# Performance work log

Hardware: AMD Instinct MI355X
Metric: run time of the kernel (lower is better)

Reference implementation:

```python
import jax, jax.numpy as jnp
import numpy as np

N_NODES = 100000
N_EDGES = 3200000
N_GRAPHS = 128
HIDDEN = 128
DEPTH = 3


def setup_inputs() -> dict:
    key = jax.random.key(0)
    ks = jax.random.split(key, 12)
    x = jax.random.normal(ks[0], (N_NODES, 1), dtype=jnp.float32)
    edge_index = jax.random.randint(ks[1], (2, N_EDGES), 0, N_NODES, dtype=jnp.int64)
    batch = jnp.sort(jax.random.randint(ks[2], (N_NODES,), 0, N_GRAPHS, dtype=jnp.int64))
    s = 1.0 / np.sqrt(HIDDEN)
    return {
        "x": x,
        "edge_index": edge_index,
        "batch": batch,
        "W_emb": jax.random.normal(ks[3], (1, HIDDEN), dtype=jnp.float32),
        "b_emb": jax.random.normal(ks[4], (HIDDEN,), dtype=jnp.float32) * 0.01,
        "W_gnn": jax.random.normal(ks[5], (DEPTH, HIDDEN, HIDDEN), dtype=jnp.float32) * s,
        "b_gnn": jax.random.normal(ks[6], (DEPTH, HIDDEN), dtype=jnp.float32) * 0.01,
        "W_c1": jax.random.normal(ks[7], (HIDDEN, HIDDEN // 2), dtype=jnp.float32) * s,
        "b_c1": jax.random.normal(ks[8], (HIDDEN // 2,), dtype=jnp.float32) * 0.01,
        "W_c2": jax.random.normal(ks[9], (HIDDEN // 2, 1), dtype=jnp.float32) * s,
        "b_c2": jax.random.normal(ks[10], (1,), dtype=jnp.float32) * 0.01,
    }


def reference(x, edge_index, batch, W_emb, b_emb, W_gnn, b_gnn, W_c1, b_c1, W_c2, b_c2):
    # --- GCN normalization (self-loops + symmetric deg^-1/2) ---
    loop = jnp.arange(N_NODES, dtype=edge_index.dtype)
    row = jnp.concatenate([edge_index[0], loop])  # source nodes
    col = jnp.concatenate([edge_index[1], loop])  # target nodes
    deg = jax.ops.segment_sum(jnp.ones_like(col, dtype=jnp.float32), col, num_segments=N_NODES)
    dinv = jnp.where(deg > 0, jax.lax.rsqrt(jnp.maximum(deg, 1.0)), 0.0)
    norm = dinv[row] * dinv[col]  # [E+N]

    # --- node embedding ---
    h = x @ W_emb + b_emb  # [N, H]

    # --- GCN layers: linear -> gather -> normalize -> scatter-add -> bias -> relu ---
    for l in range(DEPTH):
        h_lin = h @ W_gnn[l]                       # [N, H]
        msgs = h_lin[row] * norm[:, None]          # [E+N, H]
        agg = jax.ops.segment_sum(msgs, col, num_segments=N_NODES)
        h = jax.nn.relu(agg + b_gnn[l])

    # --- global mean pool per graph ---
    counts = jax.ops.segment_sum(jnp.ones((N_NODES,), jnp.float32), batch, num_segments=N_GRAPHS)
    sums = jax.ops.segment_sum(h, batch, num_segments=N_GRAPHS)
    g = sums / jnp.maximum(counts, 1.0)[:, None]   # [G, H]

    # --- classifier (dropout is identity in eval) ---
    z = jax.nn.relu(g @ W_c1 + b_c1)
    out = jax.nn.sigmoid(z @ W_c2 + b_c2)          # [G, 1]
    return out.squeeze(-1)                          # [G]
```

## Files before the change

### kernel.cpp

```cpp
#include <hip/hip_runtime.h>
#include <math.h>

#define HID 128
#define CAP 96
#define TILE 8192
#define WSH 9
#define BUKCAP 24576

typedef unsigned int uint;
typedef unsigned short ushort;
typedef float f32x2 __attribute__((ext_vector_type(2)));
typedef float f32x4 __attribute__((ext_vector_type(4)));
typedef short bf16x8 __attribute__((ext_vector_type(8)));

__device__ inline ushort f2bf(float f) {
    uint u = __float_as_uint(f);
    return (ushort)((u + 0x7fffu + ((u >> 16) & 1u)) >> 16);
}
__device__ inline float bflo(uint u) { return __uint_as_float(u << 16); }
__device__ inline float bfhi(uint u) { return __uint_as_float(u & 0xffff0000u); }
__device__ inline uint packbf(float a, float b) {
    return (uint)f2bf(a) | ((uint)f2bf(b) << 16);
}
__device__ inline bf16x8 as_bf16x8(uint4 u) {
    union { uint4 a; bf16x8 b; } c;
    c.a = u;
    return c.b;
}

__device__ inline f32x2 fp8lo(uint q) { return __builtin_amdgcn_cvt_pk_f32_fp8(q, false); }
__device__ inline f32x2 fp8hi(uint q) { return __builtin_amdgcn_cvt_pk_f32_fp8(q, true); }
__device__ inline uint pack4fp8(float a, float b, float c, float d) {
    int t = __builtin_amdgcn_cvt_pk_fp8_f32(a, b, 0, false);
    return (uint)__builtin_amdgcn_cvt_pk_fp8_f32(c, d, t, true);
}


__global__ void __launch_bounds__(256) k_part(const int* __restrict__ row,
                                              const int* __restrict__ col,
                                              int* __restrict__ bukCur,
                                              uint* __restrict__ recs, int E) {
    __shared__ int hist[256];
    __shared__ int hist2[256];
    __shared__ uint base[256];
    int t = threadIdx.x;
    hist[t] = 0;
    hist2[t] = 0;
    __syncthreads();
    int i0 = blockIdx.x * TILE;
    int i1 = min(E, i0 + TILE);
    for (int i = i0 + t; i < i1; i += 256) {
        int b = col[i] >> WSH;
        atomicAdd(&hist[b], 1);
    }
    __syncthreads();
    if (hist[t] > 0) base[t] = (uint)atomicAdd(&bukCur[t], hist[t]);
    __syncthreads();
    for (int i = i0 + t; i < i1; i += 256) {
        int c = col[i];
        int b = c >> WSH;
        uint p = (uint)atomicAdd(&hist2[b], 1);
        uint idx = base[b] + p;
        if (idx < BUKCAP)
            recs[(size_t)b * BUKCAP + idx] = (uint)row[i] | ((uint)(c & 511) << 17);
    }
}

__global__ void __launch_bounds__(256) k_fbin(const uint* __restrict__ recs,
                                              const int* __restrict__ bukCur,
                                              int* __restrict__ cnt,
                                              int* __restrict__ ebin, int N) {
    __shared__ int lcnt[512];
    int b = blockIdx.x;
    int t = threadIdx.x;
    lcnt[t] = 0;
    lcnt[t + 256] = 0;
    __syncthreads();
    int n = min(bukCur[b], BUKCAP);
    const uint* rp = recs + (size_t)b * BUKCAP;
    int cbase = b << WSH;
    for (int j = t; j < n; j += 256) {
        uint u = rp[j];
        int r = (int)(u & 0x1FFFFu);
        int cl = (int)(u >> 17);
        int p = atomicAdd(&lcnt[cl], 1);
        if (p < CAP) ebin[(size_t)(cbase + cl) * CAP + p] = r;
    }
    __syncthreads();
    int c0 = cbase + t;
    if (c0 < N) cnt[c0] = lcnt[t];
    int c1 = cbase + t + 256;
    if (c1 < N) cnt[c1] = lcnt[t + 256];
}

__global__ void k_prep(const int* __restrict__ cnt, const float* __restrict__ x,
                       float* __restrict__ dinv, float2* __restrict__ pk0, int N) {
    int i = blockIdx.x * blockDim.x + threadIdx.x;
    if (i < N) {
        float d = rsqrtf((float)cnt[i] + 1.0f);
        dinv[i] = d;
        pk0[i] = make_float2(d, d * x[i]);
    }
}


__global__ void k_uv(const float* __restrict__ W_emb, const float* __restrict__ b_emb,
                     const float* __restrict__ W0, float* __restrict__ u, float* __restrict__ v) {
    int j = threadIdx.x;
    float su = 0.f, sv = 0.f;
    for (int k = 0; k < HID; ++k) {
        float w = W0[k * HID + j];
        su = fmaf(W_emb[k], w, su);
        sv = fmaf(b_emb[k], w, sv);
    }
    u[j] = su;
    v[j] = sv;
}

__global__ void k_sagg(const int* __restrict__ cnt, const int* __restrict__ ebin,
                       const float* __restrict__ x, const float* __restrict__ dinv,
                       const float2* __restrict__ pk0,
                       float* __restrict__ s0, float* __restrict__ s1, int N) {
    int c = blockIdx.x * blockDim.x + threadIdx.x;
    if (c >= N) return;
    float dc = dinv[c];
    float A = 0.f, B = 0.f;
    int n = min(cnt[c], CAP);
    const int* bp = ebin + (size_t)c * CAP;
    int k = 0;
    for (; k + 4 <= n; k += 4) {
        float2 p0 = pk0[bp[k]], p1 = pk0[bp[k + 1]];
        float2 p2 = pk0[bp[k + 2]], p3 = pk0[bp[k + 3]];
        A += (p0.x + p1.x) + (p2.x + p3.x);
        B += (p0.y + p1.y) + (p2.y + p3.y);
    }
    for (; k < n; ++k) {
        float2 p = pk0[bp[k]];
        A += p.x;
        B += p.y;
    }
    float d2 = dc * dc;
    s0[c] = fmaf(dc, A, d2);
    s1[c] = fmaf(dc, B, d2 * x[c]);
}

__global__ void k_h1(const float* __restrict__ s0, const float* __restrict__ s1,
                     const float* __restrict__ u, const float* __restrict__ v,
                     const float* __restrict__ b0, const float* __restrict__ dinv,
                     uint* __restrict__ g8, int total) {
    int idx = blockIdx.x * blockDim.x + threadIdx.x;
    if (idx >= total) return;
    int c = idx >> 5, j = (idx & 31) * 4;
    float t0 = s1[c], t1 = s0[c];
    float dc = dinv[c];
    float v0 = fmaxf(fmaf(t0, u[j + 0], fmaf(t1, v[j + 0], b0[j + 0])), 0.f);
    float v1 = fmaxf(fmaf(t0, u[j + 1], fmaf(t1, v[j + 1], b0[j + 1])), 0.f);
    float v2 = fmaxf(fmaf(t0, u[j + 2], fmaf(t1, v[j + 2], b0[j + 2])), 0.f);
    float v3 = fmaxf(fmaf(t0, u[j + 3], fmaf(t1, v[j + 3], b0[j + 3])), 0.f);
    g8[idx] = pack4fp8(dc * v0, dc * v1, dc * v2, dc * v3);
}


__global__ void __launch_bounds__(256) k_agg(const int* __restrict__ cnt,
                                             const int* __restrict__ ebin,
                                             const float* __restrict__ dinv,
                                             const uint* __restrict__ g8,
                                             uint* __restrict__ a, int N) {
    int wave = (blockIdx.x * 256 + threadIdx.x) >> 6;
    int lane = threadIdx.x & 63;
    if (wave >= N) return;
    int c = wave;
    int sl = lane & 31;
    int halfid = lane >> 5;
    bool h0 = (halfid == 0);

    f32x2 acc01, acc23;
    {
        uint sq = g8[c * 32 + sl];
        f32x2 lo = fp8lo(sq), hi = fp8hi(sq);
        f32x2 z = {0.f, 0.f};
        acc01 = h0 ? lo : z;
        acc23 = h0 ? hi : z;
    }

    int n = min(cnt[c], CAP);
    const int* __restrict__ bp = ebin + (size_t)c * CAP;
    for (int base = 0; base < n; base += 64) {
        int cw = min(n - base, 64);
        int r = 0;
        if (lane < cw) r = bp[base + lane];
        int j = 0;
        for (; j + 8 <= cw; j += 8) {
            int rA = __shfl(r, j + halfid);
            int rB = __shfl(r, j + 2 + halfid);
            int rC = __shfl(r, j + 4 + halfid);
            int rD = __shfl(r, j + 6 + halfid);
            uint qA = g8[rA * 32 + sl];
            uint qB = g8[rB * 32 + sl];
            uint qC = g8[rC * 32 + sl];
            uint qD = g8[rD * 32 + sl];
            acc01 += fp8lo(qA); acc23 += fp8hi(qA);
            acc01 += fp8lo(qB); acc23 += fp8hi(qB);
            acc01 += fp8lo(qC); acc23 += fp8hi(qC);
            acc01 += fp8lo(qD); acc23 += fp8hi(qD);
        }
        for (; j + 2 <= cw; j += 2) {
            int rA = __shfl(r, j + halfid);
            uint qA = g8[rA * 32 + sl];
            acc01 += fp8lo(qA); acc23 += fp8hi(qA);
        }
        if (j < cw) {
            int rA = __shfl(r, j);
            uint qA = g8[rA * 32 + sl];
            if (h0) { acc01 += fp8lo(qA); acc23 += fp8hi(qA); }
        }
    }

    float a0 = acc01.x, a1 = acc01.y, a2 = acc23.x, a3 = acc23.y;
    a0 += __shfl_xor(a0, 32);
    a1 += __shfl_xor(a1, 32);
    a2 += __shfl_xor(a2, 32);
    a3 += __shfl_xor(a3, 32);
    if (h0) {
        float dc = dinv[c];
        uint2 o;
        o.x = packbf(dc * a0, dc * a1);
        o.y = packbf(dc * a2, dc * a3);
        ((uint2*)(a + (size_t)c * 64))[sl] = o;
    }
}


__global__ void k_wfrag(const float* __restrict__ W_gnn, uint4* __restrict__ wfrag) {
    int gid = blockIdx.x * 256 + threadIdx.x;
    if (gid >= 4096) return;
    int l = gid >> 11;
    int rem = gid & 2047;
    int kb = rem >> 9;
    int nt = (rem >> 6) & 7;
    int lane = rem & 63;
    int k0 = kb * 32 + (lane >> 4) * 8;
    int n = nt * 16 + (lane & 15);
    const float* Wp = W_gnn + (size_t)(l + 1) * HID * HID;
    uint4 o;
    o.x = packbf(Wp[(k0 + 0) * HID + n], Wp[(k0 + 1) * HID + n]);
    o.y = packbf(Wp[(k0 + 2) * HID + n], Wp[(k0 + 3) * HID + n]);
    o.z = packbf(Wp[(k0 + 4) * HID + n], Wp[(k0 + 5) * HID + n]);
    o.w = packbf(Wp[(k0 + 6) * HID + n], Wp[(k0 + 7) * HID + n]);
    wfrag[gid] = o;
}

#define RCH 32
__global__ void __launch_bounds__(256, 2) k_gemm(const uint* __restrict__ A,
                                                 const uint4* __restrict__ wfrag,
                                                 const float* __restrict__ bias,
                                                 const float* __restrict__ rowscale,
                                                 uint* __restrict__ H8, int N) {
    __shared__ uint4 sAf[4][2][64];
    __shared__ float sEp[4][16][68];
    int t = threadIdx.x;
    int w = t >> 6;
    int lane = t & 63;
    int rowgrp = w >> 1;
    int colh = w & 1;

    bf16x8 Bf[4][4];
#pragma unroll
    for (int kb = 0; kb < 4; ++kb)
#pragma unroll
        for (int i = 0; i < 4; ++i)
            Bf[kb][i] = as_bf16x8(wfrag[(kb * 8 + colh * 4 + i) * 64 + lane]);

    float4 bb = ((const float4*)bias)[colh * 16 + (lane & 15)];

    int nchunk = (N + RCH - 1) / RCH;
    for (int ch = blockIdx.x; ch < nchunk; ch += gridDim.x) {
        int r0 = ch * RCH;
        __syncthreads();
#pragma unroll
        for (int s = 0; s < 2; ++s) {
            int i = t + s * 256;
            int kb = i >> 7;
            int rg = (i >> 6) & 1;
            int ln = i & 63;
            int gr = r0 + rg * 16 + (ln & 15);
            gr = min(gr, N - 1);
            sAf[kb][rg][ln] = ((const uint4*)(A + (size_t)gr * 64))[kb * 4 + (ln >> 4)];
        }
        __syncthreads();

        f32x4 acc[4] = {{0.f, 0.f, 0.f, 0.f}, {0.f, 0.f, 0.f, 0.f},
                        {0.f, 0.f, 0.f, 0.f}, {0.f, 0.f, 0.f, 0.f}};
#pragma unroll
        for (int kb = 0; kb < 4; ++kb) {
            bf16x8 af = as_bf16x8(sAf[kb][rowgrp][lane]);
#pragma unroll
            for (int i = 0; i < 4; ++i)
                acc[i] = __builtin_amdgcn_mfma_f32_16x16x32_bf16(af, Bf[kb][i], acc[i], 0, 0, 0);
        }

#pragma unroll
        for (int i = 0; i < 4; ++i) {
#pragma unroll
            for (int reg = 0; reg < 4; ++reg)
                sEp[w][(lane >> 4) * 4 + reg][i * 16 + (lane & 15)] = acc[i][reg];
        }
#pragma unroll
        for (int e = 0; e < 4; ++e) {
            int rr = (lane >> 4) + 4 * e;
            int cu = lane & 15;
            const float* sp = &sEp[w][rr][cu * 4];
            int rowg = r0 + rowgrp * 16 + rr;
            if (rowg < N) {
                float sc = rowscale ? rowscale[rowg] : 1.0f;
                float o0 = sc * fmaxf(sp[0] + bb.x, 0.f);
                float o1 = sc * fmaxf(sp[1] + bb.y, 0.f);
                float o2 = sc * fmaxf(sp[2] + bb.z, 0.f);
                float o3 = sc * fmaxf(sp[3] + bb.w, 0.f);
                H8[(size_t)rowg * 32 + colh * 16 + cu] = pack4fp8(o0, o1, o2, o3);
            }
        }
    }
}


__global__ void k_pool(const uint* __restrict__ h8, const int* __restrict__ batch,
                       float* __restrict__ gpool, float* __restrict__ gcnt, int N) {
    int gi = blockIdx.x >> 2, part = blockIdx.x & 3;
    int t = threadIdx.x;
    int ui = t & 31;
    int sub = t >> 5;
    int lo = 0, hi = N;
    while (lo < hi) { int m = (lo + hi) >> 1; if (batch[m] < gi) lo = m + 1; else hi = m; }
    int start = lo;
    lo = start; hi = N;
    while (lo < hi) { int m = (lo + hi) >> 1; if (batch[m] <= gi) lo = m + 1; else hi = m; }
    int end = lo;
    if (part == 0 && t == 0) gcnt[gi] = (float)(end - start);
    int len = end - start;
    int q = (len + 15) >> 4;
    int seg = part * 4 + sub;
    int rs = start + seg * q;
    int re = min(end, rs + q);
    float s0 = 0.f, s1 = 0.f, s2 = 0.f, s3 = 0.f;
    for (int i = rs; i < re; ++i) {
        uint qq = h8[(size_t)i * 32 + ui];
        f32x2 lo2 = fp8lo(qq), hi2 = fp8hi(qq);
        s0 += lo2.x; s1 += lo2.y; s2 += hi2.x; s3 += hi2.y;
    }
    if (re > rs) {
        float* gp = gpool + gi * HID + ui * 4;
        atomicAdd(gp + 0, s0);
        atomicAdd(gp + 1, s1);
        atomicAdd(gp + 2, s2);
        atomicAdd(gp + 3, s3);
    }
}

__global__ void k_cls(const float* __restrict__ gpool, const float* __restrict__ gcnt,
                      const float* __restrict__ Wc1, const float* __restrict__ bc1,
                      const float* __restrict__ Wc2, const float* __restrict__ bc2,
                      float* __restrict__ out) {
    int g = blockIdx.x;
    int j = threadIdx.x;
    float inv = 1.0f / fmaxf(gcnt[g], 1.0f);
    float z = bc1[j];
    for (int k = 0; k < HID; ++k) z = fmaf(gpool[g * HID + k] * inv, Wc1[k * 64 + j], z);
    z = fmaxf(z, 0.f);
    float p = z * Wc2[j];
    for (int off = 32; off; off >>= 1) p += __shfl_down(p, off);
    if (j == 0) out[g] = 1.0f / (1.0f + expf(-(p + bc2[0])));
}


extern "C" void kernel_launch(void* const* d_in, const int* in_sizes, int n_in,
                              void* d_out, int out_size, void* d_ws, size_t ws_size,
                              hipStream_t stream) {
    const float* x     = (const float*)d_in[0];
    const int*   eidx  = (const int*)d_in[1];
    const int*   batch = (const int*)d_in[2];
    const float* W_emb = (const float*)d_in[3];
    const float* b_emb = (const float*)d_in[4];
    const float* W_gnn = (const float*)d_in[5];
    const float* b_gnn = (const float*)d_in[6];
    const float* W_c1  = (const float*)d_in[7];
    const float* b_c1  = (const float*)d_in[8];
    const float* W_c2  = (const float*)d_in[9];
    const float* b_c2  = (const float*)d_in[10];

    const int N = in_sizes[0];
    const int E = in_sizes[1] / 2;
    const int G = out_size;
    const int* row = eidx;
    const int* col = eidx + E;
    const int NBUK = (N + 511) >> WSH;

    char* ws = (char*)d_ws;
    auto alloc = [&](size_t bytes) -> void* {
        void* p = (void*)ws;
        ws += (bytes + 255) & ~(size_t)255;
        return p;
    };
    int*    cnt    = (int*)alloc((size_t)N * 4);
    float*  dinv   = (float*)alloc((size_t)N * 4);
    float2* pk0    = (float2*)alloc((size_t)N * 8);
    int*    bukCur = (int*)alloc(256 * 4);
    uint*   recs   = (uint*)alloc((size_t)NBUK * BUKCAP * 4);
    int*    ebin   = (int*)alloc((size_t)N * CAP * 4);
    float*  s0     = (float*)alloc((size_t)N * 4);
    float*  s1     = (float*)alloc((size_t)N * 4);
    float*  u      = (float*)alloc(HID * 4);
    float*  v      = (float*)alloc(HID * 4);
    uint*   G8     = (uint*)alloc((size_t)N * 32 * 4);
    uint*   A      = (uint*)alloc((size_t)N * 64 * 4);
    uint4*  wfrag  = (uint4*)alloc(4096 * 16);
    float*  gpool  = (float*)alloc((size_t)G * HID * 4);
    float*  gcnt   = (float*)alloc((size_t)G * 4);

    hipMemsetAsync(bukCur, 0, 256 * 4, stream);
    hipMemsetAsync(gpool, 0, (size_t)G * HID * 4, stream);

    k_part<<<(E + TILE - 1) / TILE, 256, 0, stream>>>(row, col, bukCur, recs, E);
    k_fbin<<<NBUK, 256, 0, stream>>>(recs, bukCur, cnt, ebin, N);
    k_prep<<<(N + 255) / 256, 256, 0, stream>>>(cnt, x, dinv, pk0, N);

    k_uv<<<1, HID, 0, stream>>>(W_emb, b_emb, W_gnn, u, v);
    k_sagg<<<(N + 255) / 256, 256, 0, stream>>>(cnt, ebin, x, dinv, pk0, s0, s1, N);
    k_h1<<<(N * 32 + 255) / 256, 256, 0, stream>>>(s0, s1, u, v, b_gnn, dinv, G8, N * 32);

    k_wfrag<<<16, 256, 0, stream>>>(W_gnn, wfrag);

    int nchunk = (N + RCH - 1) / RCH;
    int gblk = nchunk < 768 ? nchunk : 768;
    for (int l = 1; l < 3; ++l) {
        k_agg<<<(N + 3) / 4, 256, 0, stream>>>(cnt, ebin, dinv, G8, A, N);
        k_gemm<<<gblk, 256, 0, stream>>>(A, wfrag + (size_t)(l - 1) * 2048,
                                         b_gnn + (size_t)l * HID,
                                         (l == 1) ? dinv : (const float*)nullptr,
                                         G8, N);
    }

    k_pool<<<G * 4, 128, 0, stream>>>(G8, batch, gpool, gcnt, N);
    k_cls<<<G, 64, 0, stream>>>(gpool, gcnt, W_c1, b_c1, W_c2, b_c2, (float*)d_out);
}
```

Baseline: 381.0 us.

## Fuse prep kernels, precompute scaled gather offsets, and drop pooling atomics

Folds degree normalization into the binning kernel, merges the weight-fragment and u/v precompute into one launch, and fuses the scalar aggregation with layer-1 feature generation through shared memory. Edge bins now hold source indices pre-shifted by 5, so the aggregation loop skips a multiply per gather. Pooling uses one block per graph with a shared-memory reduction and plain stores, which removes atomics and the gpool memset. Together these cut several launches and intermediate arrays; the trade-off is less parallelism in pooling (128 blocks instead of 512).

Measured after the change: 411.6 us. 1.08x slower.

```diff
diff --git a/kernel.cpp b/kernel.cpp
--- a/kernel.cpp
+++ b/kernel.cpp
@@ -17,8 +17,6 @@
     uint u = __float_as_uint(f);
     return (ushort)((u + 0x7fffu + ((u >> 16) & 1u)) >> 16);
 }
-__device__ inline float bflo(uint u) { return __uint_as_float(u << 16); }
-__device__ inline float bfhi(uint u) { return __uint_as_float(u & 0xffff0000u); }
 __device__ inline uint packbf(float a, float b) {
     return (uint)f2bf(a) | ((uint)f2bf(b) << 16);
 }
@@ -68,8 +66,11 @@
 
 __global__ void __launch_bounds__(256) k_fbin(const uint* __restrict__ recs,
                                               const int* __restrict__ bukCur,
+                                              const float* __restrict__ x,
                                               int* __restrict__ cnt,
-                                              int* __restrict__ ebin, int N) {
+                                              int* __restrict__ ebin,
+                                              float* __restrict__ dinv,
+                                              float2* __restrict__ pk0, int N) {
     __shared__ int lcnt[512];
     int b = blockIdx.x;
     int t = threadIdx.x;
@@ -84,80 +85,109 @@
         int r = (int)(u & 0x1FFFFu);
         int cl = (int)(u >> 17);
         int p = atomicAdd(&lcnt[cl], 1);
-        if (p < CAP) ebin[(size_t)(cbase + cl) * CAP + p] = r;
+        if (p < CAP) ebin[(size_t)(cbase + cl) * CAP + p] = r << 5;
     }
     __syncthreads();
     int c0 = cbase + t;
-    if (c0 < N) cnt[c0] = lcnt[t];
+    if (c0 < N) {
+        cnt[c0] = lcnt[t];
+        float d = rsqrtf((float)lcnt[t] + 1.0f);
+        dinv[c0] = d;
+        pk0[c0] = make_float2(d, d * x[c0]);
+    }
     int c1 = cbase + t + 256;
-    if (c1 < N) cnt[c1] = lcnt[t + 256];
-}
-
-__global__ void k_prep(const int* __restrict__ cnt, const float* __restrict__ x,
-                       float* __restrict__ dinv, float2* __restrict__ pk0, int N) {
-    int i = blockIdx.x * blockDim.x + threadIdx.x;
-    if (i < N) {
-        float d = rsqrtf((float)cnt[i] + 1.0f);
-        dinv[i] = d;
-        pk0[i] = make_float2(d, d * x[i]);
-    }
-}
-
-
-__global__ void k_uv(const float* __restrict__ W_emb, const float* __restrict__ b_emb,
-                     const float* __restrict__ W0, float* __restrict__ u, float* __restrict__ v) {
-    int j = threadIdx.x;
-    float su = 0.f, sv = 0.f;
-    for (int k = 0; k < HID; ++k) {
-        float w = W0[k * HID + j];
-        su = fmaf(W_emb[k], w, su);
-        sv = fmaf(b_emb[k], w, sv);
-    }
-    u[j] = su;
-    v[j] = sv;
-}
-
-__global__ void k_sagg(const int* __restrict__ cnt, const int* __restrict__ ebin,
-                       const float* __restrict__ x, const float* __restrict__ dinv,
-                       const float2* __restrict__ pk0,
-                       float* __restrict__ s0, float* __restrict__ s1, int N) {
-    int c = blockIdx.x * blockDim.x + threadIdx.x;
-    if (c >= N) return;
-    float dc = dinv[c];
-    float A = 0.f, B = 0.f;
-    int n = min(cnt[c], CAP);
-    const int* bp = ebin + (size_t)c * CAP;
-    int k = 0;
-    for (; k + 4 <= n; k += 4) {
-        float2 p0 = pk0[bp[k]], p1 = pk0[bp[k + 1]];
-        float2 p2 = pk0[bp[k + 2]], p3 = pk0[bp[k + 3]];
-        A += (p0.x + p1.x) + (p2.x + p3.x);
-        B += (p0.y + p1.y) + (p2.y + p3.y);
-    }
-    for (; k < n; ++k) {
-        float2 p = pk0[bp[k]];
-        A += p.x;
-        B += p.y;
-    }
-    float d2 = dc * dc;
-    s0[c] = fmaf(dc, A, d2);
-    s1[c] = fmaf(dc, B, d2 * x[c]);
-}
-
-__global__ void k_h1(const float* __restrict__ s0, const float* __restrict__ s1,
-                     const float* __restrict__ u, const float* __restrict__ v,
-                     const float* __restrict__ b0, const float* __restrict__ dinv,
-                     uint* __restrict__ g8, int total) {
-    int idx = blockIdx.x * blockDim.x + threadIdx.x;
-    if (idx >= total) return;
-    int c = idx >> 5, j = (idx & 31) * 4;
-    float t0 = s1[c], t1 = s0[c];
-    float dc = dinv[c];
-    float v0 = fmaxf(fmaf(t0, u[j + 0], fmaf(t1, v[j + 0], b0[j + 0])), 0.f);
-    float v1 = fmaxf(fmaf(t0, u[j + 1], fmaf(t1, v[j + 1], b0[j + 1])), 0.f);
-    float v2 = fmaxf(fmaf(t0, u[j + 2], fmaf(t1, v[j + 2], b0[j + 2])), 0.f);
-    float v3 = fmaxf(fmaf(t0, u[j + 3], fmaf(t1, v[j + 3], b0[j + 3])), 0.f);
-    g8[idx] = pack4fp8(dc * v0, dc * v1, dc * v2, dc * v3);
+    if (c1 < N) {
+        cnt[c1] = lcnt[t + 256];
+        float d = rsqrtf((float)lcnt[t + 256] + 1.0f);
+        dinv[c1] = d;
+        pk0[c1] = make_float2(d, d * x[c1]);
+    }
+}
+
+
+__global__ void k_wprep(const float* __restrict__ W_emb, const float* __restrict__ b_emb,
+                        const float* __restrict__ W_gnn,
+                        float* __restrict__ u, float* __restrict__ v,
+                        uint4* __restrict__ wfrag) {
+    int b = blockIdx.x;
+    int t = threadIdx.x;
+    if (b < 16) {
+        int gid = b * 256 + t;
+        int l = gid >> 11;
+        int rem = gid & 2047;
+        int kb = rem >> 9;
+        int nt = (rem >> 6) & 7;
+        int lane = rem & 63;
+        int k0 = kb * 32 + (lane >> 4) * 8;
+        int n = nt * 16 + (lane & 15);
+        const float* Wp = W_gnn + (size_t)(l + 1) * HID * HID;
+        uint4 o;
+        o.x = packbf(Wp[(k0 + 0) * HID + n], Wp[(k0 + 1) * HID + n]);
+        o.y = packbf(Wp[(k0 + 2) * HID + n], Wp[(k0 + 3) * HID + n]);
+        o.z = packbf(Wp[(k0 + 4) * HID + n], Wp[(k0 + 5) * HID + n]);
+        o.w = packbf(Wp[(k0 + 6) * HID + n], Wp[(k0 + 7) * HID + n]);
+        wfrag[gid] = o;
+    } else if (t < HID) {
+        float su = 0.f, sv = 0.f;
+        for (int k = 0; k < HID; ++k) {
+            float w = W_gnn[k * HID + t];
+            su = fmaf(W_emb[k], w, su);
+            sv = fmaf(b_emb[k], w, sv);
+        }
+        u[t] = su;
+        v[t] = sv;
+    }
+}
+
+
+__global__ void __launch_bounds__(256) k_sagg(const int* __restrict__ cnt,
+                                              const int* __restrict__ ebin,
+                                              const float* __restrict__ x,
+                                              const float* __restrict__ dinv,
+                                              const float2* __restrict__ pk0,
+                                              const float* __restrict__ u,
+                                              const float* __restrict__ v,
+                                              const float* __restrict__ b0,
+                                              uint* __restrict__ g8, int N) {
+    __shared__ float sS0[256], sS1[256], sDc[256];
+    int t = threadIdx.x;
+    int c0 = blockIdx.x * 256;
+    int c = c0 + t;
+    if (c < N) {
+        float dc = dinv[c];
+        float A = 0.f, B = 0.f;
+        int n = min(cnt[c], CAP);
+        const int* bp = ebin + (size_t)c * CAP;
+        int k = 0;
+        for (; k + 4 <= n; k += 4) {
+            float2 p0 = pk0[bp[k] >> 5], p1 = pk0[bp[k + 1] >> 5];
+            float2 p2 = pk0[bp[k + 2] >> 5], p3 = pk0[bp[k + 3] >> 5];
+            A += (p0.x + p1.x) + (p2.x + p3.x);
+            B += (p0.y + p1.y) + (p2.y + p3.y);
+        }
+        for (; k < n; ++k) {
+            float2 p = pk0[bp[k] >> 5];
+            A += p.x;
+            B += p.y;
+        }
+        float d2 = dc * dc;
+        sS0[t] = fmaf(dc, A, d2);
+        sS1[t] = fmaf(dc, B, d2 * x[c]);
+        sDc[t] = dc;
+    }
+    __syncthreads();
+    int nloc = min(256, N - c0);
+    int total = nloc * 32;
+    for (int gid = t; gid < total; gid += 256) {
+        int lc = gid >> 5;
+        int j = (gid & 31) * 4;
+        float t1 = sS1[lc], t0 = sS0[lc], dc = sDc[lc];
+        float v0 = fmaxf(fmaf(t1, u[j + 0], fmaf(t0, v[j + 0], b0[j + 0])), 0.f);
+        float v1 = fmaxf(fmaf(t1, u[j + 1], fmaf(t0, v[j + 1], b0[j + 1])), 0.f);
+        float v2 = fmaxf(fmaf(t1, u[j + 2], fmaf(t0, v[j + 2], b0[j + 2])), 0.f);
+        float v3 = fmaxf(fmaf(t1, u[j + 3], fmaf(t0, v[j + 3], b0[j + 3])), 0.f);
+        g8[(size_t)(c0 + lc) * 32 + (gid & 31)] = pack4fp8(dc * v0, dc * v1, dc * v2, dc * v3);
+    }
 }
 
 
@@ -187,31 +217,31 @@
     const int* __restrict__ bp = ebin + (size_t)c * CAP;
     for (int base = 0; base < n; base += 64) {
         int cw = min(n - base, 64);
-        int r = 0;
-        if (lane < cw) r = bp[base + lane];
+        int ro = 0;
+        if (lane < cw) ro = bp[base + lane];
         int j = 0;
         for (; j + 8 <= cw; j += 8) {
-            int rA = __shfl(r, j + halfid);
-            int rB = __shfl(r, j + 2 + halfid);
-            int rC = __shfl(r, j + 4 + halfid);
-            int rD = __shfl(r, j + 6 + halfid);
-            uint qA = g8[rA * 32 + sl];
-            uint qB = g8[rB * 32 + sl];
-            uint qC = g8[rC * 32 + sl];
-            uint qD = g8[rD * 32 + sl];
+            int oA = __shfl(ro, j + halfid);
+            int oB = __shfl(ro, j + 2 + halfid);
+            int oC = __shfl(ro, j + 4 + halfid);
+            int oD = __shfl(ro, j + 6 + halfid);
+            uint qA = g8[oA + sl];
+            uint qB = g8[oB + sl];
+            uint qC = g8[oC + sl];
+            uint qD = g8[oD + sl];
             acc01 += fp8lo(qA); acc23 += fp8hi(qA);
             acc01 += fp8lo(qB); acc23 += fp8hi(qB);
             acc01 += fp8lo(qC); acc23 += fp8hi(qC);
             acc01 += fp8lo(qD); acc23 += fp8hi(qD);
         }
         for (; j + 2 <= cw; j += 2) {
-            int rA = __shfl(r, j + halfid);
-            uint qA = g8[rA * 32 + sl];
+            int oA = __shfl(ro, j + halfid);
+            uint qA = g8[oA + sl];
             acc01 += fp8lo(qA); acc23 += fp8hi(qA);
         }
         if (j < cw) {
-            int rA = __shfl(r, j);
-            uint qA = g8[rA * 32 + sl];
+            int oA = __shfl(ro, j);
+            uint qA = g8[oA + sl];
             if (h0) { acc01 += fp8lo(qA); acc23 += fp8hi(qA); }
         }
     }
@@ -230,25 +260,6 @@
     }
 }
 
-
-__global__ void k_wfrag(const float* __restrict__ W_gnn, uint4* __restrict__ wfrag) {
-    int gid = blockIdx.x * 256 + threadIdx.x;
-    if (gid >= 4096) return;
-    int l = gid >> 11;
-    int rem = gid & 2047;
-    int kb = rem >> 9;
-    int nt = (rem >> 6) & 7;
-    int lane = rem & 63;
-    int k0 = kb * 32 + (lane >> 4) * 8;
-    int n = nt * 16 + (lane & 15);
-    const float* Wp = W_gnn + (size_t)(l + 1) * HID * HID;
-    uint4 o;
-    o.x = packbf(Wp[(k0 + 0) * HID + n], Wp[(k0 + 1) * HID + n]);
-    o.y = packbf(Wp[(k0 + 2) * HID + n], Wp[(k0 + 3) * HID + n]);
-    o.z = packbf(Wp[(k0 + 4) * HID + n], Wp[(k0 + 5) * HID + n]);
-    o.w = packbf(Wp[(k0 + 6) * HID + n], Wp[(k0 + 7) * HID + n]);
-    wfrag[gid] = o;
-}
 
 #define RCH 32
 __global__ void __launch_bounds__(256, 2) k_gemm(const uint* __restrict__ A,
@@ -324,37 +335,43 @@
 }
 
 
-__global__ void k_pool(const uint* __restrict__ h8, const int* __restrict__ batch,
-                       float* __restrict__ gpool, float* __restrict__ gcnt, int N) {
-    int gi = blockIdx.x >> 2, part = blockIdx.x & 3;
+__global__ void __launch_bounds__(128) k_pool(const uint* __restrict__ h8,
+                                              const int* __restrict__ batch,
+                                              float* __restrict__ gpool,
+                                              float* __restrict__ gcnt, int N) {
+    __shared__ float red[4][32][4];
+    int g = blockIdx.x;
     int t = threadIdx.x;
     int ui = t & 31;
     int sub = t >> 5;
     int lo = 0, hi = N;
-    while (lo < hi) { int m = (lo + hi) >> 1; if (batch[m] < gi) lo = m + 1; else hi = m; }
+    while (lo < hi) { int m = (lo + hi) >> 1; if (batch[m] < g) lo = m + 1; else hi = m; }
     int start = lo;
     lo = start; hi = N;
-    while (lo < hi) { int m = (lo + hi) >> 1; if (batch[m] <= gi) lo = m + 1; else hi = m; }
+    while (lo < hi) { int m = (lo + hi) >> 1; if (batch[m] <= g) lo = m + 1; else hi = m; }
     int end = lo;
-    if (part == 0 && t == 0) gcnt[gi] = (float)(end - start);
-    int len = end - start;
-    int q = (len + 15) >> 4;
-    int seg = part * 4 + sub;
-    int rs = start + seg * q;
-    int re = min(end, rs + q);
     float s0 = 0.f, s1 = 0.f, s2 = 0.f, s3 = 0.f;
-    for (int i = rs; i < re; ++i) {
+    for (int i = start + sub; i < end; i += 4) {
         uint qq = h8[(size_t)i * 32 + ui];
         f32x2 lo2 = fp8lo(qq), hi2 = fp8hi(qq);
         s0 += lo2.x; s1 += lo2.y; s2 += hi2.x; s3 += hi2.y;
     }
-    if (re > rs) {
-        float* gp = gpool + gi * HID + ui * 4;
-        atomicAdd(gp + 0, s0);
-        atomicAdd(gp + 1, s1);
-        atomicAdd(gp + 2, s2);
-        atomicAdd(gp + 3, s3);
-    }
+    red[sub][ui][0] = s0;
+    red[sub][ui][1] = s1;
+    red[sub][ui][2] = s2;
+    red[sub][ui][3] = s3;
+    __syncthreads();
+    if (sub == 0) {
+        for (int k = 1; k < 4; ++k) {
+            s0 += red[k][ui][0];
+            s1 += red[k][ui][1];
+            s2 += red[k][ui][2];
+            s3 += red[k][ui][3];
+        }
+        float* gp = gpool + g * HID + ui * 4;
+        gp[0] = s0; gp[1] = s1; gp[2] = s2; gp[3] = s3;
+    }
+    if (t == 0) gcnt[g] = (float)(end - start);
 }
 
 __global__ void k_cls(const float* __restrict__ gpool, const float* __restrict__ gcnt,
@@ -407,8 +424,6 @@
     int*    bukCur = (int*)alloc(256 * 4);
     uint*   recs   = (uint*)alloc((size_t)NBUK * BUKCAP * 4);
     int*    ebin   = (int*)alloc((size_t)N * CAP * 4);
-    float*  s0     = (float*)alloc((size_t)N * 4);
-    float*  s1     = (float*)alloc((size_t)N * 4);
     float*  u      = (float*)alloc(HID * 4);
     float*  v      = (float*)alloc(HID * 4);
     uint*   G8     = (uint*)alloc((size_t)N * 32 * 4);
@@ -418,17 +433,13 @@
     float*  gcnt   = (float*)alloc((size_t)G * 4);
 
     hipMemsetAsync(bukCur, 0, 256 * 4, stream);
-    hipMemsetAsync(gpool, 0, (size_t)G * HID * 4, stream);
 
     k_part<<<(E + TILE - 1) / TILE, 256, 0, stream>>>(row, col, bukCur, recs, E);
-    k_fbin<<<NBUK, 256, 0, stream>>>(recs, bukCur, cnt, ebin, N);
-    k_prep<<<(N + 255) / 256, 256, 0, stream>>>(cnt, x, dinv, pk0, N);
-
-    k_uv<<<1, HID, 0, stream>>>(W_emb, b_emb, W_gnn, u, v);
-    k_sagg<<<(N + 255) / 256, 256, 0, stream>>>(cnt, ebin, x, dinv, pk0, s0, s1, N);
-    k_h1<<<(N * 32 + 255) / 256, 256, 0, stream>>>(s0, s1, u, v, b_gnn, dinv, G8, N * 32);
-
-    k_wfrag<<<16, 256, 0, stream>>>(W_gnn, wfrag);
+    k_fbin<<<NBUK, 256, 0, stream>>>(recs, bukCur, x, cnt, ebin, dinv, pk0, N);
+
+    k_wprep<<<17, 256, 0, stream>>>(W_emb, b_emb, W_gnn, u, v, wfrag);
+
+    k_sagg<<<(N + 255) / 256, 256, 0, stream>>>(cnt, ebin, x, dinv, pk0, u, v, b_gnn, G8, N);
 
     int nchunk = (N + RCH - 1) / RCH;
     int gblk = nchunk < 768 ? nchunk : 768;
@@ -440,6 +451,6 @@
                                          G8, N);
     }
 
-    k_pool<<<G * 4, 128, 0, stream>>>(G8, batch, gpool, gcnt, N);
+    k_pool<<<G, 128, 0, stream>>>(G8, batch, gpool, gcnt, N);
     k_cls<<<G, 64, 0, stream>>>(gpool, gcnt, W_c1, b_c1, W_c2, b_c2, (float*)d_out);
 }
```
